# Kernel optimization log

Measured on AMD Instinct MI355X. Metric: run time of the kernel, lower is better.

The kernel has to match this reference:

```python
import jax, jax.numpy as jnp
import numpy as np

PHI = (1.0 + 5.0 ** 0.5) / 2.0
TWO_PI = 2.0 * np.pi
LN_EPS = 1e-5


def _complex_linear(xr, xi, Wr, Wi, br, bi):
    # (Wr + i*Wi) @ (xr + i*xi) + (br + i*bi)
    yr = xr @ Wr.T - xi @ Wi.T + br
    yi = xr @ Wi.T + xi @ Wr.T + bi
    return yr, yi


def _layernorm(x, g, b):
    m = jnp.mean(x, axis=-1, keepdims=True)
    v = jnp.mean((x - m) ** 2, axis=-1, keepdims=True)
    return (x - m) * jax.lax.rsqrt(v + LN_EPS) * g + b


def reference(w, b, ip_Wr, ip_Wi, ip_br, ip_bi, ln_g, ln_b, W_qkv, log_alpha, op_Wr, op_Wi):
    B, S, D = w.shape
    H = log_alpha.shape[0]
    Dh = D // H
    scale = jnp.sqrt(jnp.asarray(Dh, w.dtype))
    alpha = jax.nn.sigmoid(log_alpha)[None, :, None]  # (1,H,1)
    ts = jnp.arange(S, dtype=w.dtype)

    def step(carry, xs):
        hr, hi, vs = carry          # (B,D),(B,D),(B,H,Dh)
        w_t, b_t, t = xs            # (B,D),(B,D),()
        # InstrumentedEulerTransform: separated theta, complex product
        wl = 1.0 + jnp.abs(w_t)
        tphi = (t * PHI) % TWO_PI   # wrap_time_periodic
        thr = hr / wl + b_t + tphi
        thi = hi / wl + b_t + tphi
        sr, cr = jnp.sin(thr), jnp.cos(thr)
        si, ci = jnp.sin(thi), jnp.cos(thi)
        hr2 = cr * ci - sr * si
        hi2 = cr * si + sr * ci
        # InstrumentedEchoChamber.forward_step
        pr, pi_ = _complex_linear(hr2, hi2, ip_Wr, ip_Wi, ip_br, ip_bi)
        xc = _layernorm(pr + pi_, ln_g, ln_b)
        qkv = (xc @ W_qkv.T).reshape(B, 3, H, Dh)
        q, k, v = qkv[:, 0], qkv[:, 1], qkv[:, 2]
        vs2 = alpha * v + (1.0 - alpha) * vs
        gate = jax.nn.sigmoid(jnp.sum(q * k, axis=-1, keepdims=True) / scale)
        retr = (gate * vs2).reshape(B, D)
        # output_proj ComplexLinear on (retr, 0), no bias
        ore = retr @ op_Wr.T
        oim = retr @ op_Wi.T
        return (hr2, hi2, vs2), (ore, oim)

    init = (jnp.zeros((B, D), w.dtype), jnp.zeros((B, D), w.dtype),
            jnp.zeros((B, H, Dh), w.dtype))
    wT = jnp.swapaxes(w, 0, 1)  # (S,B,D)
    bT = jnp.swapaxes(b, 0, 1)
    _, (or_seq, oi_seq) = jax.lax.scan(step, init, (wT, bT, ts))
    out = jnp.stack([or_seq, oi_seq])      # (2,S,B,D)
    return jnp.swapaxes(out, 1, 2)         # (2,B,S,D)


def setup_inputs() -> dict:
    key = jax.random.key(0)
    ks = jax.random.split(key, 10)
    B, S, D, H = 8, 2048, 512, 8
    s = 0.02
    return {
        "w": jax.random.normal(ks[0], (B, S, D), jnp.float32),
        "b": jax.random.normal(ks[1], (B, S, D), jnp.float32),
        "ip_Wr": jax.random.normal(ks[2], (D, D), jnp.float32) * s,
        "ip_Wi": jax.random.normal(ks[3], (D, D), jnp.float32) * s,
        "ip_br": jax.random.normal(ks[4], (D,), jnp.float32) * s,
        "ip_bi": jax.random.normal(ks[5], (D,), jnp.float32) * s,
        "ln_g": jnp.ones((D,), jnp.float32),
        "ln_b": jnp.zeros((D,), jnp.float32),
        "W_qkv": jax.random.normal(ks[6], (3 * D, D), jnp.float32) * s,
        "log_alpha": jax.random.normal(ks[7], (H,), jnp.float32),
        "op_Wr": jax.random.normal(ks[8], (D, D), jnp.float32) * s,
        "op_Wi": jax.random.normal(ks[9], (D, D), jnp.float32) * s,
    }
```

## Files before the change

kernel.cpp:

```cpp
#include <hip/hip_runtime.h>
#include <math.h>

#define BB 8
#define SS 2048
#define DD 512
#define HH 8
#define MM (BB*SS)

#define CHK 128
#define CL  16
#define CW  32

#define RT 64
#define RW 96

typedef unsigned short u16;
typedef unsigned int   u32;
typedef float f32x4 __attribute__((ext_vector_type(4)));
typedef short s16x8 __attribute__((ext_vector_type(8)));

__device__ __forceinline__ u16 f2bf(float x){
  union { float f; unsigned u; } c; c.f = x;
  unsigned r = c.u + 0x7FFF + ((c.u >> 16) & 1);
  return (u16)(r >> 16);
}
__device__ __forceinline__ float bf2f(u16 x){
  union { unsigned u; float f; } c; c.u = ((unsigned)x) << 16;
  return c.f;
}
__device__ __forceinline__ void gload16(const u16* g, u16* l){
  __builtin_amdgcn_global_load_lds(
      (const __attribute__((address_space(1))) unsigned int*)g,
      (__attribute__((address_space(3))) unsigned int*)l, 16, 0, 0);
}

__global__ void prep_all(const float* __restrict__ ipWr, const float* __restrict__ ipWi,
                         const float* __restrict__ Wqkv,
                         const float* __restrict__ opWr, const float* __restrict__ opWi,
                         const float* __restrict__ ipbr, const float* __restrict__ ipbi,
                         const float* __restrict__ la,
                         const float* __restrict__ lng, const float* __restrict__ lnb,
                         u16* __restrict__ W1, u16* __restrict__ Wq, u16* __restrict__ W3,
                         float* __restrict__ tphi2, float* __restrict__ bc,
                         float* __restrict__ alph,
                         float* __restrict__ c1v, float* __restrict__ c2v){
  int id = blockIdx.x*256 + threadIdx.x;
  if (id < 524288){
    int e = id & 7, lane = (id>>3) & 63, s = (id>>9) & 3;
    int rest = id >> 11, ks = rest & 31, nb2 = rest >> 5;
    int n = (nb2>>1)*128 + (nb2&1)*64 + s*16 + (lane&15);
    int k = ks*32 + (lane>>4)*8 + e;
    int d = k >> 1;
    float v = (k & 1) ? (ipWr[n*512+d] - ipWi[n*512+d])
                      : (ipWr[n*512+d] + ipWi[n*512+d]);
    W1[id] = f2bf(v);
  } else if (id < 1310720){
    int i = id - 524288;
    int e = i & 7, lane = (i>>3) & 63, s = (i>>9) & 3;
    int rest = i >> 11, ks = rest & 15, nb2 = rest >> 4;
    int n = (nb2>>1)*128 + (nb2&1)*64 + s*16 + (lane&15);
    int k = ks*32 + (lane>>4)*8 + e;
    Wq[i] = f2bf(Wqkv[n*512+k] * lng[k]);
  } else if (id < 1835008){
    int i = id - 1310720;
    int e = i & 7, lane = (i>>3) & 63, s = (i>>9) & 3;
    int rest = i >> 11, ks = rest & 15, nb2 = rest >> 4;
    int n = (nb2>>1)*128 + (nb2&1)*64 + s*16 + (lane&15);
    int k = ks*32 + (lane>>4)*8 + e;
    W3[i] = f2bf((n < 512) ? opWr[n*512+k] : opWi[(n-512)*512+k]);
  } else if (id < 1837056){
    int t = id - 1835008;
    const float PHI_F    = 1.61803398874989484820f;
    const float TWO_PI_F = 6.28318530717958647693f;
    tphi2[t] = 2.0f * fmodf((float)t * PHI_F, TWO_PI_F);
  } else if (id < 1837568){
    int t = id - 1837056;
    bc[t] = ipbr[t] + ipbi[t];
  } else if (id < 1837576){
    int t = id - 1837568;
    alph[t] = 1.0f/(1.0f + expf(-la[t]));
  } else if (id < 1839112){
    int n = id - 1837576;
    const float* wrow = Wqkv + (size_t)n*512;
    float sc1 = 0.f, sc2 = 0.f;
    for (int k=0;k<512;k++){
      float wv = wrow[k];
      sc1 = fmaf(lng[k], wv, sc1);
      sc2 = fmaf(lnb[k], wv, sc2);
    }
    c1v[n] = sc1; c2v[n] = sc2;
  }
}

__global__ __launch_bounds__(256) void stats_final(const float* __restrict__ Pst,
                                                   float* __restrict__ murs){
  int r = blockIdx.x*256 + threadIdx.x;
  const float4* p = (const float4*)(Pst + (size_t)r*16);
  float4 a = p[0], b = p[1], c = p[2], d = p[3];
  float s  = a.x+a.z + b.x+b.z + c.x+c.z + d.x+d.z;
  float s2 = a.y+a.w + b.y+b.w + c.y+c.w + d.y+d.w;
  float mu  = s  * (1.0f/512.0f);
  float var = s2 * (1.0f/512.0f) - mu*mu;
  murs[r*2]   = mu;
  murs[r*2+1] = rsqrtf(var + 1e-5f);
}

__global__ __launch_bounds__(256) void scan_h(const float* __restrict__ w,
                                              const float* __restrict__ bb,
                                              const float* __restrict__ tphi2,
                                              u32* __restrict__ X32){
  const int e = blockIdx.x*256 + threadIdx.x;
  const int c = blockIdx.y;
  const int b = e >> 9;
  const int d = e & 511;
  const float SQRT2 = 1.41421356237309504880f;
  const float PI_4  = 0.78539816339744830962f;
  const int tstart = c*CL;
  int t0 = tstart - CW; if (t0 < 0) t0 = 0;
  const int nw = tstart - t0;

  const float* wp = w  + ((size_t)b*SS + t0)*DD + d;
  const float* bp = bb + ((size_t)b*SS + t0)*DD + d;
  const float* tp = tphi2 + t0;

  const int U = 8;
  float wv[U], bv[U], wn[U], bn[U];

  float ss = 0.f;
  const int ngw = nw >> 3;
  if (ngw > 0){
    #pragma unroll
    for (int i=0;i<U;i++){ wv[i] = wp[(size_t)i*DD]; bv[i] = bp[(size_t)i*DD]; }
    for (int gg=0; gg<ngw; ++gg){
      if (gg+1 < ngw){
        const float* wnp = wp + (size_t)(gg+1)*U*DD;
        const float* bnp = bp + (size_t)(gg+1)*U*DD;
        #pragma unroll
        for (int i=0;i<U;i++){ wn[i] = wnp[(size_t)i*DD]; bn[i] = bnp[(size_t)i*DD]; }
      }
      #pragma unroll
      for (int i=0;i<U;i++){
        float rwl2 = SQRT2 * __builtin_amdgcn_rcpf(1.0f + fabsf(wv[i]));
        float cw   = fmaf(2.0f, bv[i], tp[gg*U+i]) + PI_4;
        ss = __sinf(fmaf(ss, rwl2, cw));
      }
      #pragma unroll
      for (int i=0;i<U;i++){ wv[i]=wn[i]; bv[i]=bn[i]; }
    }
  }
  float hs = SQRT2 * ss;

  const float* wq = wp + (size_t)nw*DD;
  const float* bq = bp + (size_t)nw*DD;
  const float* tq = tp + nw;
  u32* xp = X32 + (size_t)(b*SS + tstart)*512 + d;

  #pragma unroll
  for (int i=0;i<U;i++){ wv[i] = wq[(size_t)i*DD]; bv[i] = bq[(size_t)i*DD]; }
  for (int gg=0; gg<CL/U; ++gg){
    if (gg+1 < CL/U){
      const float* wnp = wq + (size_t)(gg+1)*U*DD;
      const float* bnp = bq + (size_t)(gg+1)*U*DD;
      #pragma unroll
      for (int i=0;i<U;i++){ wn[i] = wnp[(size_t)i*DD]; bn[i] = bnp[(size_t)i*DD]; }
    }
    #pragma unroll
    for (int i=0;i<U;i++){
      float rwl = __builtin_amdgcn_rcpf(1.0f + fabsf(wv[i]));
      float cc  = fmaf(2.0f, bv[i], tq[gg*U+i]);
      float theta = fmaf(hs, rwl, cc);
      float sn = __sinf(theta);
      float cs = __cosf(theta);
      hs = cs + sn;
      xp[(size_t)(gg*U+i)*512] = (u32)f2bf(cs) | ((u32)f2bf(sn) << 16);
    }
    #pragma unroll
    for (int i=0;i<U;i++){ wv[i]=wn[i]; bv[i]=bn[i]; }
  }
}

template<int TAG, int EPI>
__global__ __launch_bounds__(256) void gemm_bf16(const u16* __restrict__ A,
                                                 const u16* __restrict__ W,
                                                 float* __restrict__ C0,
                                                 float* __restrict__ C1,
                                                 u16* __restrict__ C2,
                                                 const float* __restrict__ bias,
                                                 const float* __restrict__ murs,
                                                 const float* __restrict__ c1v,
                                                 const float* __restrict__ c2v,
                                                 float* __restrict__ Pst,
                                                 int N, int K){
  __shared__ __align__(16) u16 As[3][128*32];
  const int tid  = threadIdx.x;
  const int nwgx = gridDim.x;
  const int nwg  = nwgx * gridDim.y;
  const int lin  = blockIdx.y * nwgx + blockIdx.x;
  const int qq   = nwg >> 3;
  const int logi = (lin & 7) * qq + (lin >> 3);
  const int m0   = (logi / nwgx) * 128;
  const int n0   = (logi % nwgx) * 128;

  const int wave = tid >> 6;
  const int lane = tid & 63;
  const int wr   = wave >> 1, wc = wave & 1;
  const int l15  = lane & 15;
  const int g    = lane >> 4;

  const int rI   = lane >> 2;
  const int kgs  = (lane & 3) ^ ((lane >> 3) & 3);
  const int row0 = wave*32 + rI;
  const int row1 = wave*32 + 16 + rI;
  const u16* Asrc0 = A + (size_t)(m0 + row0) * K + kgs*8;
  const u16* Asrc1 = A + (size_t)(m0 + row1) * K + kgs*8;
  const int ld0 = (wave*2+0)*512;
  const int ld1 = (wave*2+1)*512;

  const int nK = K >> 5;
  const u16* Bf = W + ((size_t)((n0 >> 6) + wc) * nK) * 2048 + lane*8;

  f32x4 acc[4][4];
  #pragma unroll
  for (int i=0;i<4;i++)
    #pragma unroll
    for (int j=0;j<4;j++) acc[i][j] = (f32x4){0.f,0.f,0.f,0.f};

  s16x8 b0[4], b1[4];

#define STAGE_A(buf, koff) do {                    \
    gload16(Asrc0 + (koff), &As[buf][ld0]);        \
    gload16(Asrc1 + (koff), &As[buf][ld1]);        \
  } while(0)

#define LOADB(dst, hh) do {                                         \
    _Pragma("unroll")                                               \
    for (int s=0;s<4;s++)                                           \
      dst[s] = *(const s16x8*)(Bf + ((size_t)(hh)*4 + s)*512);      \
  } while(0)

#define PHASE(hh, bcur, bnxt) do {                                       \
    if ((hh)+2 < nK){                                                    \
      int nb = (hh)+2; nb -= (nb/3)*3;                                   \
      STAGE_A(nb, ((hh)+2)*32);                                          \
    }                                                                    \
    if ((hh)+1 < nK) LOADB(bnxt, (hh)+1);                                \
    {                                                                    \
      int rem = nK - 1 - (hh);                                           \
      if      (rem >= 2) asm volatile("s_waitcnt vmcnt(6)" ::: "memory");\
      else if (rem == 1) asm volatile("s_waitcnt vmcnt(4)" ::: "memory");\
      else               asm volatile("s_waitcnt vmcnt(0)" ::: "memory");\
    }                                                                    \
    __builtin_amdgcn_s_barrier();        \
    {                                                                    \
      int cb = (hh); cb -= (cb/3)*3;                                     \
      const u16* Ah = &As[cb][0];                                        \
      s16x8 af[4];                                                       \
      _Pragma("unroll")                                                  \
      for (int s=0;s<4;s++){                                             \
        int rA = wr*64 + s*16 + l15;                                     \
        af[s] = *(const s16x8*)&Ah[rA*32 + ((g ^ ((rA>>1)&3))*8)];       \
      }                                                                  \
      __builtin_amdgcn_s_setprio(1);                                     \
      _Pragma("unroll")                                                  \
      for (int mi=0;mi<4;mi++)                                           \
        _Pragma("unroll")                                                \
        for (int ni=0;ni<4;ni++)                                         \
          acc[mi][ni] = __builtin_amdgcn_mfma_f32_16x16x32_bf16(af[mi], bcur[ni], acc[mi][ni], 0, 0, 0); \
      __builtin_amdgcn_s_setprio(0);                                     \
    }                                                                    \
    asm volatile("" ::: "memory");                                       \
    __builtin_amdgcn_s_barrier();        \
  } while(0)

  STAGE_A(0, 0);
  STAGE_A(1, 32);
  LOADB(b0, 0);

  for (int h = 0; h < nK; h += 2){
    PHASE(h,   b0, b1);
    PHASE(h+1, b1, b0);
  }

#undef STAGE_A
#undef LOADB
#undef PHASE

  #pragma unroll
  for (int mi=0;mi<4;mi++){
    #pragma unroll
    for (int j=0;j<4;j++){
      int r = m0 + wr*64 + mi*16 + g*4 + j;
      if (EPI == 1){
        #pragma unroll
        for (int ni=0;ni<4;ni++){
          int col = n0 + wc*64 + ni*16 + l15;
          float v = acc[mi][ni][j];
          if (col < 512) C0[(size_t)r*512 + col]       = v;
          else           C1[(size_t)r*512 + (col-512)] = v;
        }
      } else if (EPI == 3){
        float s1 = 0.f, s2v = 0.f;
        #pragma unroll
        for (int ni=0;ni<4;ni++){
          int col = n0 + wc*64 + ni*16 + l15;
          float v = acc[mi][ni][j] + bias[col];
          C2[(size_t)r*N + col] = f2bf(v);
          s1 += v; s2v = fmaf(v, v, s2v);
        }
        #pragma unroll
        for (int off=1; off<16; off<<=1){
          s1  += __shfl_xor(s1,  off);
          s2v += __shfl_xor(s2v, off);
        }
        if (l15 == 0){
          int slice = (n0 >> 6) + wc;
          Pst[((size_t)r*8 + slice)*2]     = s1;
          Pst[((size_t)r*8 + slice)*2 + 1] = s2v;
        }
      } else {
        float mu = murs[r*2], rs = murs[r*2+1];
        #pragma unroll
        for (int ni=0;ni<4;ni++){
          int col = n0 + wc*64 + ni*16 + l15;
          float v = rs*(acc[mi][ni][j] - mu*c1v[col]) + c2v[col];
          C2[(size_t)r*N + col] = f2bf(v);
        }
      }
    }
  }
}

__global__ __launch_bounds__(256) void retr_fused(const u16* __restrict__ qkv,
                                                  const float* __restrict__ alph,
                                                  u16* __restrict__ retr){
  const int wid  = blockIdx.x*4 + (threadIdx.x >> 6);
  const int lane = threadIdx.x & 63;
  const int c = wid & 31;
  const int h = (wid >> 5) & 7;
  const int b = wid >> 8;
  const float a  = alph[h];
  const float om = 1.0f - a;
  const int d  = h*64 + lane;
  const int t0 = c*RT;
  int w0 = t0 - RW; if (w0 < 0) w0 = 0;
  const int nw = t0 - w0;

  const u16* vp = qkv + ((size_t)(b*SS + w0))*1536 + 1024 + d;
  float vs = 0.f;
  {
    const int U = 8;
    float vv[U], vn[U];
    const int ng = nw >> 3;
    if (ng > 0){
      #pragma unroll
      for (int i=0;i<U;i++) vv[i] = bf2f(vp[(size_t)i*1536]);
      for (int gg=0; gg<ng; ++gg){
        if (gg+1 < ng){
          const u16* vnp = vp + (size_t)(gg+1)*U*1536;
          #pragma unroll
          for (int i=0;i<U;i++) vn[i] = bf2f(vnp[(size_t)i*1536]);
        }
        #pragma unroll
        for (int i=0;i<U;i++) vs = fmaf(a, vv[i], om*vs);
        #pragma unroll
        for (int i=0;i<U;i++) vv[i] = vn[i];
      }
    }
  }
  const u16* qp = qkv + ((size_t)(b*SS + t0))*1536 + d;
  u16* op = retr + ((size_t)(b*SS + t0))*512 + d;
  #pragma unroll 4
  for (int i=0;i<RT;i++){
    float q  = bf2f(qp[(size_t)i*1536]);
    float kk = bf2f(qp[(size_t)i*1536 + 512]);
    float v  = bf2f(qp[(size_t)i*1536 + 1024]);
    vs = fmaf(a, v, om*vs);
    float p = q*kk;
    #pragma unroll
    for (int off=32; off>0; off>>=1) p += __shfl_xor(p, off);
    float gate = 1.0f/(1.0f + __expf(-p*0.125f));
    op[(size_t)i*512] = f2bf(gate * vs);
  }
}

extern "C" void kernel_launch(void* const* d_in, const int* in_sizes, int n_in,
                              void* d_out, int out_size, void* d_ws, size_t ws_size,
                              hipStream_t stream) {
  const float* w    = (const float*)d_in[0];
  const float* b    = (const float*)d_in[1];
  const float* ipWr = (const float*)d_in[2];
  const float* ipWi = (const float*)d_in[3];
  const float* ipbr = (const float*)d_in[4];
  const float* ipbi = (const float*)d_in[5];
  const float* lng  = (const float*)d_in[6];
  const float* lnb  = (const float*)d_in[7];
  const float* Wqkv = (const float*)d_in[8];
  const float* la   = (const float*)d_in[9];
  const float* opWr = (const float*)d_in[10];
  const float* opWi = (const float*)d_in[11];
  float* out0 = (float*)d_out;
  float* out1 = out0 + (size_t)MM*DD;

  char* base = (char*)d_ws;
  u16*   W1    = (u16*)  (base + 0);
  u16*   Wq    = (u16*)  (base + 1048576);
  u16*   W3    = (u16*)  (base + 2621440);
  float* bc    = (float*)(base + 3670016);
  float* alph  = (float*)(base + 3672064);
  float* tphi2 = (float*)(base + 3672128);
  u32*   X32   = (u32*)  (base + 3680384);
  u16*   y     = (u16*)  (base + 37234816);
  u16*   qkv   = (u16*)  (base + 70789248);
  float* c1v   = (float*)(base + 121120896);
  float* c2v   = (float*)(base + 121127040);
  float* murs  = (float*)(base + 121133184);
  float* Pst   = (float*)(base + 121264256);
  u16*   retr  = (u16*)X32;

  prep_all<<<7184,256,0,stream>>>(ipWr, ipWi, Wqkv, opWr, opWi, ipbr, ipbi, la,
                                  lng, lnb, W1, Wq, W3, tphi2, bc, alph, c1v, c2v);

  scan_h<<<dim3(16,CHK),256,0,stream>>>(w, b, tphi2, X32);

  gemm_bf16<1,3><<<dim3(4,128),256,0,stream>>>((const u16*)X32, W1, nullptr, nullptr, y,
                                               bc, nullptr, nullptr, nullptr, Pst, 512, 1024);
  stats_final<<<64,256,0,stream>>>(Pst, murs);
  gemm_bf16<2,4><<<dim3(12,128),256,0,stream>>>(y, Wq, nullptr, nullptr, qkv,
                                                nullptr, murs, c1v, c2v, nullptr, 1536, 512);

  retr_fused<<<512,256,0,stream>>>(qkv, alph, retr);

  gemm_bf16<3,1><<<dim3(8,128),256,0,stream>>>(retr, W3, out0, out1, nullptr,
                                               nullptr, nullptr, nullptr, nullptr, nullptr, 1024, 512);
}
```

Measured before the change: 173.0 us.

## Fuse q·k head dot product into QKV GEMM epilogue and split V GEMM

Q and K weight rows are interleaved per head so the q·k gate reduction happens in the GEMM epilogue, which writes only a per-row, per-head float. V gets its own GEMM, so the full bf16 q/k tensors are never written out or reread by the retrieval kernel. Scan chunking also changes (fewer chunks, longer chunks), and the GEMM template becomes macro-based specialized kernels with K fixed at compile time. This trades an extra kernel launch and shared-memory reduction for much less memory traffic. Precision shifts slightly because q and k are not rounded to bf16 before the product.

```diff
diff --git a/kernel.cpp b/kernel.cpp
--- a/kernel.cpp
+++ b/kernel.cpp
@@ -7,8 +7,8 @@
 #define HH 8
 #define MM (BB*SS)
 
-#define CHK 128
-#define CL  16
+#define CHK 64
+#define CL  32
 #define CW  32
 
 #define RT 64
@@ -40,9 +40,11 @@
                          const float* __restrict__ ipbr, const float* __restrict__ ipbi,
                          const float* __restrict__ la,
                          const float* __restrict__ lng, const float* __restrict__ lnb,
-                         u16* __restrict__ W1, u16* __restrict__ Wq, u16* __restrict__ W3,
+                         u16* __restrict__ W1, u16* __restrict__ Wqk, u16* __restrict__ Wv,
+                         u16* __restrict__ W3,
                          float* __restrict__ tphi2, float* __restrict__ bc,
                          float* __restrict__ alph,
+                         float* __restrict__ c1qk, float* __restrict__ c2qk,
                          float* __restrict__ c1v, float* __restrict__ c2v){
   int id = blockIdx.x*256 + threadIdx.x;
   if (id < 524288){
@@ -54,13 +56,22 @@
     float v = (k & 1) ? (ipWr[n*512+d] - ipWi[n*512+d])
                       : (ipWr[n*512+d] + ipWi[n*512+d]);
     W1[id] = f2bf(v);
-  } else if (id < 1310720){
+  } else if (id < 1048576){
     int i = id - 524288;
     int e = i & 7, lane = (i>>3) & 63, s = (i>>9) & 3;
     int rest = i >> 11, ks = rest & 15, nb2 = rest >> 4;
     int n = (nb2>>1)*128 + (nb2&1)*64 + s*16 + (lane&15);
     int k = ks*32 + (lane>>4)*8 + e;
-    Wq[i] = f2bf(Wqkv[n*512+k] * lng[k]);
+    int head = n >> 7, idx = n & 127;
+    int orig = head*64 + (idx>>1) + ((idx&1) ? 512 : 0);
+    Wqk[i] = f2bf(Wqkv[(size_t)orig*512 + k] * lng[k]);
+  } else if (id < 1310720){
+    int i = id - 1048576;
+    int e = i & 7, lane = (i>>3) & 63, s = (i>>9) & 3;
+    int rest = i >> 11, ks = rest & 15, nb2 = rest >> 4;
+    int n = (nb2>>1)*128 + (nb2&1)*64 + s*16 + (lane&15);
+    int k = ks*32 + (lane>>4)*8 + e;
+    Wv[i] = f2bf(Wqkv[(size_t)(1024+n)*512 + k] * lng[k]);
   } else if (id < 1835008){
     int i = id - 1310720;
     int e = i & 7, lane = (i>>3) & 63, s = (i>>9) & 3;
@@ -79,16 +90,28 @@
   } else if (id < 1837576){
     int t = id - 1837568;
     alph[t] = 1.0f/(1.0f + expf(-la[t]));
-  } else if (id < 1839112){
+  } else if (id < 1838600){
     int n = id - 1837576;
-    const float* wrow = Wqkv + (size_t)n*512;
-    float sc1 = 0.f, sc2 = 0.f;
+    int head = n >> 7, idx = n & 127;
+    int orig = head*64 + (idx>>1) + ((idx&1) ? 512 : 0);
+    const float* wrow = Wqkv + (size_t)orig*512;
+    float s1 = 0.f, s2 = 0.f;
     for (int k=0;k<512;k++){
       float wv = wrow[k];
-      sc1 = fmaf(lng[k], wv, sc1);
-      sc2 = fmaf(lnb[k], wv, sc2);
-    }
-    c1v[n] = sc1; c2v[n] = sc2;
+      s1 = fmaf(lng[k], wv, s1);
+      s2 = fmaf(lnb[k], wv, s2);
+    }
+    c1qk[n] = s1; c2qk[n] = s2;
+  } else if (id < 1839112){
+    int n = id - 1838600;
+    const float* wrow = Wqkv + (size_t)(1024+n)*512;
+    float s1 = 0.f, s2 = 0.f;
+    for (int k=0;k<512;k++){
+      float wv = wrow[k];
+      s1 = fmaf(lng[k], wv, s1);
+      s2 = fmaf(lnb[k], wv, s2);
+    }
+    c1v[n] = s1; c2v[n] = s2;
   }
 }
 
@@ -179,52 +202,34 @@
   }
 }
 
-template<int TAG, int EPI>
-__global__ __launch_bounds__(256) void gemm_bf16(const u16* __restrict__ A,
-                                                 const u16* __restrict__ W,
-                                                 float* __restrict__ C0,
-                                                 float* __restrict__ C1,
-                                                 u16* __restrict__ C2,
-                                                 const float* __restrict__ bias,
-                                                 const float* __restrict__ murs,
-                                                 const float* __restrict__ c1v,
-                                                 const float* __restrict__ c2v,
-                                                 float* __restrict__ Pst,
-                                                 int N, int K){
-  __shared__ __align__(16) u16 As[3][128*32];
-  const int tid  = threadIdx.x;
-  const int nwgx = gridDim.x;
-  const int nwg  = nwgx * gridDim.y;
-  const int lin  = blockIdx.y * nwgx + blockIdx.x;
-  const int qq   = nwg >> 3;
-  const int logi = (lin & 7) * qq + (lin >> 3);
-  const int m0   = (logi / nwgx) * 128;
-  const int n0   = (logi % nwgx) * 128;
-
-  const int wave = tid >> 6;
-  const int lane = tid & 63;
-  const int wr   = wave >> 1, wc = wave & 1;
-  const int l15  = lane & 15;
-  const int g    = lane >> 4;
-
-  const int rI   = lane >> 2;
-  const int kgs  = (lane & 3) ^ ((lane >> 3) & 3);
-  const int row0 = wave*32 + rI;
-  const int row1 = wave*32 + 16 + rI;
-  const u16* Asrc0 = A + (size_t)(m0 + row0) * K + kgs*8;
-  const u16* Asrc1 = A + (size_t)(m0 + row1) * K + kgs*8;
-  const int ld0 = (wave*2+0)*512;
-  const int ld1 = (wave*2+1)*512;
-
-  const int nK = K >> 5;
-  const u16* Bf = W + ((size_t)((n0 >> 6) + wc) * nK) * 2048 + lane*8;
-
-  f32x4 acc[4][4];
-  #pragma unroll
-  for (int i=0;i<4;i++)
-    #pragma unroll
-    for (int j=0;j<4;j++) acc[i][j] = (f32x4){0.f,0.f,0.f,0.f};
-
+#define GEMM_PRE(KDIM)                                                   \
+  const int K = KDIM, nK = KDIM >> 5;                                    \
+  __shared__ __align__(16) u16 As[3][128*32];                            \
+  const int tid  = threadIdx.x;                                          \
+  const int nwgx = gridDim.x;                                            \
+  const int nwg  = nwgx * gridDim.y;                                     \
+  const int lin  = blockIdx.y * nwgx + blockIdx.x;                       \
+  const int qq   = nwg >> 3;                                             \
+  const int logi = (lin & 7) * qq + (lin >> 3);                          \
+  const int m0   = (logi / nwgx) * 128;                                  \
+  const int n0   = (logi % nwgx) * 128;                                  \
+  const int wave = tid >> 6;                                             \
+  const int lane = tid & 63;                                             \
+  const int wr   = wave >> 1, wc = wave & 1;                             \
+  const int l15  = lane & 15;                                            \
+  const int g    = lane >> 4;                                            \
+  const int rI   = lane >> 2;                                            \
+  const int kgs  = (lane & 3) ^ ((lane >> 3) & 3);                       \
+  const u16* Asrc0 = A + (size_t)(m0 + wave*32 + rI) * K + kgs*8;        \
+  const u16* Asrc1 = A + (size_t)(m0 + wave*32 + 16 + rI) * K + kgs*8;   \
+  const int ld0 = (wave*2+0)*512;                                        \
+  const int ld1 = (wave*2+1)*512;                                        \
+  const u16* Bf = W + ((size_t)((n0 >> 6) + wc) * nK) * 2048 + lane*8;   \
+  f32x4 acc[4][4];                                                       \
+  _Pragma("unroll")                                                      \
+  for (int i=0;i<4;i++)                                                  \
+    _Pragma("unroll")                                                    \
+    for (int j=0;j<4;j++) acc[i][j] = (f32x4){0.f,0.f,0.f,0.f};          \
   s16x8 b0[4], b1[4];
 
 #define STAGE_A(buf, koff) do {                    \
@@ -250,7 +255,7 @@
       else if (rem == 1) asm volatile("s_waitcnt vmcnt(4)" ::: "memory");\
       else               asm volatile("s_waitcnt vmcnt(0)" ::: "memory");\
     }                                                                    \
-    __builtin_amdgcn_s_barrier();        \
+    __builtin_amdgcn_s_barrier();                                        \
     {                                                                    \
       int cb = (hh); cb -= (cb/3)*3;                                     \
       const u16* Ah = &As[cb][0];                                        \
@@ -269,68 +274,137 @@
       __builtin_amdgcn_s_setprio(0);                                     \
     }                                                                    \
     asm volatile("" ::: "memory");                                       \
-    __builtin_amdgcn_s_barrier();        \
+    __builtin_amdgcn_s_barrier();                                        \
   } while(0)
 
-  STAGE_A(0, 0);
-  STAGE_A(1, 32);
-  LOADB(b0, 0);
-
-  for (int h = 0; h < nK; h += 2){
-    PHASE(h,   b0, b1);
-    PHASE(h+1, b1, b0);
-  }
-
-#undef STAGE_A
-#undef LOADB
-#undef PHASE
-
+#define GEMM_LOOP                                  \
+  STAGE_A(0, 0);                                   \
+  STAGE_A(1, 32);                                  \
+  LOADB(b0, 0);                                    \
+  for (int h = 0; h < nK; h += 2){                 \
+    PHASE(h,   b0, b1);                            \
+    PHASE(h+1, b1, b0);                            \
+  }
+
+__global__ __launch_bounds__(256) void gemm_y(const u16* __restrict__ A,
+                                              const u16* __restrict__ W,
+                                              u16* __restrict__ Y,
+                                              const float* __restrict__ bias,
+                                              float* __restrict__ Pst){
+  GEMM_PRE(1024)
+  GEMM_LOOP
   #pragma unroll
   for (int mi=0;mi<4;mi++){
     #pragma unroll
     for (int j=0;j<4;j++){
       int r = m0 + wr*64 + mi*16 + g*4 + j;
-      if (EPI == 1){
-        #pragma unroll
-        for (int ni=0;ni<4;ni++){
-          int col = n0 + wc*64 + ni*16 + l15;
-          float v = acc[mi][ni][j];
-          if (col < 512) C0[(size_t)r*512 + col]       = v;
-          else           C1[(size_t)r*512 + (col-512)] = v;
-        }
-      } else if (EPI == 3){
-        float s1 = 0.f, s2v = 0.f;
-        #pragma unroll
-        for (int ni=0;ni<4;ni++){
-          int col = n0 + wc*64 + ni*16 + l15;
-          float v = acc[mi][ni][j] + bias[col];
-          C2[(size_t)r*N + col] = f2bf(v);
-          s1 += v; s2v = fmaf(v, v, s2v);
-        }
-        #pragma unroll
-        for (int off=1; off<16; off<<=1){
-          s1  += __shfl_xor(s1,  off);
-          s2v += __shfl_xor(s2v, off);
-        }
-        if (l15 == 0){
-          int slice = (n0 >> 6) + wc;
-          Pst[((size_t)r*8 + slice)*2]     = s1;
-          Pst[((size_t)r*8 + slice)*2 + 1] = s2v;
-        }
-      } else {
-        float mu = murs[r*2], rs = murs[r*2+1];
-        #pragma unroll
-        for (int ni=0;ni<4;ni++){
-          int col = n0 + wc*64 + ni*16 + l15;
-          float v = rs*(acc[mi][ni][j] - mu*c1v[col]) + c2v[col];
-          C2[(size_t)r*N + col] = f2bf(v);
-        }
-      }
-    }
-  }
-}
-
-__global__ __launch_bounds__(256) void retr_fused(const u16* __restrict__ qkv,
+      float s1 = 0.f, s2v = 0.f;
+      #pragma unroll
+      for (int ni=0;ni<4;ni++){
+        int col = n0 + wc*64 + ni*16 + l15;
+        float vv = acc[mi][ni][j] + bias[col];
+        Y[(size_t)r*512 + col] = f2bf(vv);
+        s1 += vv; s2v = fmaf(vv, vv, s2v);
+      }
+      #pragma unroll
+      for (int off=1; off<16; off<<=1){
+        s1  += __shfl_xor(s1,  off);
+        s2v += __shfl_xor(s2v, off);
+      }
+      if (l15 == 0){
+        int slice = (n0 >> 6) + wc;
+        Pst[((size_t)r*8 + slice)*2]     = s1;
+        Pst[((size_t)r*8 + slice)*2 + 1] = s2v;
+      }
+    }
+  }
+}
+
+__global__ __launch_bounds__(256) void gemm_qk(const u16* __restrict__ A,
+                                               const u16* __restrict__ W,
+                                               const float* __restrict__ murs,
+                                               const float* __restrict__ c1,
+                                               const float* __restrict__ c2,
+                                               float* __restrict__ QK){
+  __shared__ float qkp[2][128];
+  GEMM_PRE(512)
+  GEMM_LOOP
+  const int head = n0 >> 7;
+  #pragma unroll
+  for (int mi=0;mi<4;mi++){
+    #pragma unroll
+    for (int j=0;j<4;j++){
+      int r = m0 + wr*64 + mi*16 + g*4 + j;
+      float mu = murs[r*2], rs = murs[r*2+1];
+      float p = 0.f;
+      #pragma unroll
+      for (int ni=0;ni<4;ni++){
+        int col = n0 + wc*64 + ni*16 + l15;
+        float vv = rs*(acc[mi][ni][j] - mu*c1[col]) + c2[col];
+        float pv = __shfl_xor(vv, 1);
+        p = fmaf(vv, pv, p);
+      }
+      p += __shfl_xor(p, 2);
+      p += __shfl_xor(p, 4);
+      p += __shfl_xor(p, 8);
+      if (l15 == 0) qkp[wc][wr*64 + mi*16 + g*4 + j] = p;
+    }
+  }
+  __syncthreads();
+  if (tid < 128){
+    float s = qkp[0][tid] + qkp[1][tid];
+    QK[(size_t)(m0 + tid)*8 + head] = s;
+  }
+}
+
+__global__ __launch_bounds__(256) void gemm_v(const u16* __restrict__ A,
+                                              const u16* __restrict__ W,
+                                              const float* __restrict__ murs,
+                                              const float* __restrict__ c1,
+                                              const float* __restrict__ c2,
+                                              u16* __restrict__ V){
+  GEMM_PRE(512)
+  GEMM_LOOP
+  #pragma unroll
+  for (int mi=0;mi<4;mi++){
+    #pragma unroll
+    for (int j=0;j<4;j++){
+      int r = m0 + wr*64 + mi*16 + g*4 + j;
+      float mu = murs[r*2], rs = murs[r*2+1];
+      #pragma unroll
+      for (int ni=0;ni<4;ni++){
+        int col = n0 + wc*64 + ni*16 + l15;
+        float vv = rs*(acc[mi][ni][j] - mu*c1[col]) + c2[col];
+        V[(size_t)r*512 + col] = f2bf(vv);
+      }
+    }
+  }
+}
+
+__global__ __launch_bounds__(256) void gemm_out(const u16* __restrict__ A,
+                                                const u16* __restrict__ W,
+                                                float* __restrict__ C0,
+                                                float* __restrict__ C1){
+  GEMM_PRE(512)
+  GEMM_LOOP
+  #pragma unroll
+  for (int mi=0;mi<4;mi++){
+    #pragma unroll
+    for (int j=0;j<4;j++){
+      int r = m0 + wr*64 + mi*16 + g*4 + j;
+      #pragma unroll
+      for (int ni=0;ni<4;ni++){
+        int col = n0 + wc*64 + ni*16 + l15;
+        float v = acc[mi][ni][j];
+        if (col < 512) C0[(size_t)r*512 + col]       = v;
+        else           C1[(size_t)r*512 + (col-512)] = v;
+      }
+    }
+  }
+}
+
+__global__ __launch_bounds__(256) void retr_fused(const u16* __restrict__ v,
+                                                  const float* __restrict__ QK,
                                                   const float* __restrict__ alph,
                                                   u16* __restrict__ retr){
   const int wid  = blockIdx.x*4 + (threadIdx.x >> 6);
@@ -345,7 +419,7 @@
   int w0 = t0 - RW; if (w0 < 0) w0 = 0;
   const int nw = t0 - w0;
 
-  const u16* vp = qkv + ((size_t)(b*SS + w0))*1536 + 1024 + d;
+  const u16* vp = v + ((size_t)(b*SS + w0))*512 + d;
   float vs = 0.f;
   {
     const int U = 8;
@@ -353,12 +427,12 @@
     const int ng = nw >> 3;
     if (ng > 0){
       #pragma unroll
-      for (int i=0;i<U;i++) vv[i] = bf2f(vp[(size_t)i*1536]);
+      for (int i=0;i<U;i++) vv[i] = bf2f(vp[(size_t)i*512]);
       for (int gg=0; gg<ng; ++gg){
         if (gg+1 < ng){
-          const u16* vnp = vp + (size_t)(gg+1)*U*1536;
+          const u16* vnp = vp + (size_t)(gg+1)*U*512;
           #pragma unroll
-          for (int i=0;i<U;i++) vn[i] = bf2f(vnp[(size_t)i*1536]);
+          for (int i=0;i<U;i++) vn[i] = bf2f(vnp[(size_t)i*512]);
         }
         #pragma unroll
         for (int i=0;i<U;i++) vs = fmaf(a, vv[i], om*vs);
@@ -367,18 +441,15 @@
       }
     }
   }
-  const u16* qp = qkv + ((size_t)(b*SS + t0))*1536 + d;
+  const u16* qp = v + ((size_t)(b*SS + t0))*512 + d;
+  const float* gp = QK + ((size_t)(b*SS + t0))*8 + h;
   u16* op = retr + ((size_t)(b*SS + t0))*512 + d;
   #pragma unroll 4
   for (int i=0;i<RT;i++){
-    float q  = bf2f(qp[(size_t)i*1536]);
-    float kk = bf2f(qp[(size_t)i*1536 + 512]);
-    float v  = bf2f(qp[(size_t)i*1536 + 1024]);
-    vs = fmaf(a, v, om*vs);
-    float p = q*kk;
-    #pragma unroll
-    for (int off=32; off>0; off>>=1) p += __shfl_xor(p, off);
-    float gate = 1.0f/(1.0f + __expf(-p*0.125f));
+    float vv = bf2f(qp[(size_t)i*512]);
+    vs = fmaf(a, vv, om*vs);
+    float qk = gp[(size_t)i*8];
+    float gate = 1.0f/(1.0f + __expf(-qk*0.125f));
     op[(size_t)i*512] = f2bf(gate * vs);
   }
 }
@@ -403,33 +474,37 @@
 
   char* base = (char*)d_ws;
   u16*   W1    = (u16*)  (base + 0);
-  u16*   Wq    = (u16*)  (base + 1048576);
+  u16*   Wqk   = (u16*)  (base + 1048576);
+  u16*   Wv    = (u16*)  (base + 2097152);
   u16*   W3    = (u16*)  (base + 2621440);
   float* bc    = (float*)(base + 3670016);
   float* alph  = (float*)(base + 3672064);
   float* tphi2 = (float*)(base + 3672128);
-  u32*   X32   = (u32*)  (base + 3680384);
-  u16*   y     = (u16*)  (base + 37234816);
-  u16*   qkv   = (u16*)  (base + 70789248);
-  float* c1v   = (float*)(base + 121120896);
-  float* c2v   = (float*)(base + 121127040);
-  float* murs  = (float*)(base + 121133184);
-  float* Pst   = (float*)(base + 121264256);
+  float* c1qk  = (float*)(base + 3680384);
+  float* c2qk  = (float*)(base + 3684480);
+  float* c1v   = (float*)(base + 3688576);
+  float* c2v   = (float*)(base + 3690624);
+  float* murs  = (float*)(base + 3692672);
+  float* Pst   = (float*)(base + 3823744);
+  u32*   X32   = (u32*)  (base + 4872320);
+  u16*   y     = (u16*)  (base + 38426752);
+  u16*   v     = (u16*)  (base + 55203968);
+  float* QK    = (float*)(base + 71981184);
   u16*   retr  = (u16*)X32;
 
-  prep_all<<<7184,256,0,stream>>>(ipWr, ipWi, Wqkv, opWr, opWi, ipbr, ipbi, la,
-                                  lng, lnb, W1, Wq, W3, tphi2, bc, alph, c1v, c2v);
+  prep_all<<<7185,256,0,stream>>>(ipWr, ipWi, Wqkv, opWr, opWi, ipbr, ipbi, la,
+                                  lng, lnb, W1, Wqk, Wv, W3, tphi2, bc, alph,
+                                  c1qk, c2qk, c1v, c2v);
 
   scan_h<<<dim3(16,CHK),256,0,stream>>>(w, b, tphi2, X32);
 
-  gemm_bf16<1,3><<<dim3(4,128),256,0,stream>>>((const u16*)X32, W1, nullptr, nullptr, y,
-                                               bc, nullptr, nullptr, nullptr, Pst, 512, 1024);
+  gemm_y<<<dim3(4,128),256,0,stream>>>((const u16*)X32, W1, y, bc, Pst);
   stats_final<<<64,256,0,stream>>>(Pst, murs);
-  gemm_bf16<2,4><<<dim3(12,128),256,0,stream>>>(y, Wq, nullptr, nullptr, qkv,
-                                                nullptr, murs, c1v, c2v, nullptr, 1536, 512);
-
-  retr_fused<<<512,256,0,stream>>>(qkv, alph, retr);
-
-  gemm_bf16<3,1><<<dim3(8,128),256,0,stream>>>(retr, W3, out0, out1, nullptr,
-                                               nullptr, nullptr, nullptr, nullptr, nullptr, 1024, 512);
-}
+
+  gemm_qk<<<dim3(8,128),256,0,stream>>>(y, Wqk, murs, c1qk, c2qk, QK);
+  gemm_v<<<dim3(4,128),256,0,stream>>>(y, Wv, murs, c1v, c2v, v);
+
+  retr_fused<<<512,256,0,stream>>>(v, QK, alph, retr);
+
+  gemm_out<<<dim3(8,128),256,0,stream>>>(retr, W3, out0, out1);
+}
```

Result: no change. 170.8 us (-1.3%).
